# Kernel tuning notes

Measured on AMD Instinct MI355X. Metric: run time of the kernel, lower is better.

## Reference

```python
import jax, jax.numpy as jnp
import numpy as np

FEATURE_DIM = 256
NUM_STEPS = 3
NUM_GRAPHS = 2048
ATOMS_PER_GRAPH = 64
TOTAL_ATOMS = NUM_GRAPHS * ATOMS_PER_GRAPH


def setup_inputs() -> dict:
    key = jax.random.key(0)
    k_x, k1, k2, k3, k4 = jax.random.split(key, 5)
    H = FEATURE_DIM
    s = 1.0 / np.sqrt(H)
    x = jax.random.normal(k_x, (TOTAL_ATOMS, H), dtype=jnp.float32)
    batch = jnp.repeat(jnp.arange(NUM_GRAPHS, dtype=jnp.int64), ATOMS_PER_GRAPH)
    sizes = jnp.full((NUM_GRAPHS,), ATOMS_PER_GRAPH, dtype=jnp.int64)
    # LSTM params (PyTorch layout: gates ordered i, f, g, o)
    W_ih = jax.random.uniform(k1, (4 * H, H), jnp.float32, -s, s)
    W_hh = jax.random.uniform(k2, (4 * H, H), jnp.float32, -s, s)
    b_ih = jax.random.uniform(k3, (4 * H,), jnp.float32, -s, s)
    b_hh = jax.random.uniform(k4, (4 * H,), jnp.float32, -s, s)
    return {"x": x, "batch": batch, "sizes": sizes,
            "W_ih": W_ih, "W_hh": W_hh, "b_ih": b_ih, "b_hh": b_hh}


def _lstm_cell(u, hx, cx, W_ih, W_hh, b_ih, b_hh):
    # u: input [B,H]; (hx, cx): hidden/cell [B,H]
    gates = u @ W_ih.T + b_ih + hx @ W_hh.T + b_hh  # [B, 4H]
    i, f, g, o = jnp.split(gates, 4, axis=-1)
    i, f, o = jax.nn.sigmoid(i), jax.nn.sigmoid(f), jax.nn.sigmoid(o)
    c = f * cx + i * jnp.tanh(g)
    h = o * jnp.tanh(c)
    return h, c


def _segment_softmax(scores, seg, num_segments):
    m = jax.ops.segment_max(scores, seg, num_segments=num_segments)
    e = jnp.exp(scores - m[seg])
    s = jax.ops.segment_sum(e, seg, num_segments=num_segments)
    return e / s[seg]


def reference(x, batch, sizes, W_ih, W_hh, b_ih, b_hh):
    B = sizes.shape[0]
    H = x.shape[1]
    seg = batch.astype(jnp.int32)
    h = jnp.zeros((B, H), dtype=x.dtype)
    c = jnp.zeros((B, H), dtype=x.dtype)
    q = h
    r = h
    for _ in range(NUM_STEPS):
        # torch code feeds h both as LSTM input and hidden state
        q, c = _lstm_cell(h, h, c, W_ih, W_hh, b_ih, b_hh)
        scores = jnp.sum(x * q[seg], axis=-1)              # [total_atoms]
        attn = _segment_softmax(scores, seg, B)            # per-graph softmax
        r = jax.ops.segment_sum(x * attn[:, None], seg, num_segments=B)  # [B,H]
        h = r  # torch code overwrites the LSTM hidden with r
    return jnp.concatenate([q, r], axis=-1)  # [B, 2H]
```

## Files before the change

kernel.cpp:

```cpp
#include <hip/hip_runtime.h>
#include <math.h>

#define H 256
#define NB 2048
#define APG 64

typedef __attribute__((ext_vector_type(8))) short short8;
typedef __attribute__((ext_vector_type(4))) float f32x4;

__device__ __forceinline__ unsigned short f2bf(float f) {
    unsigned u = __float_as_uint(f);
    u += 0x7fff + ((u >> 16) & 1);
    return (unsigned short)(u >> 16);
}
__device__ __forceinline__ float bf2f(unsigned short s) {
    return __uint_as_float((unsigned)s << 16);
}
__device__ __forceinline__ float sigm(float v) { return 1.f / (1.f + __expf(-v)); }

__global__ void prep_kernel(const float* __restrict__ W_ih, const float* __restrict__ W_hh,
                            const float* __restrict__ b_ih, const float* __restrict__ b_hh,
                            unsigned short* __restrict__ Wr, float* __restrict__ br) {
    int idx = blockIdx.x * 256 + threadIdx.x;
    int wr_row = idx >> 8, k = idx & 255;
    int hcol = wr_row >> 2, gate = wr_row & 3;
    int src = gate * 65536 + hcol * 256 + k;
    Wr[idx] = f2bf(W_ih[src] + W_hh[src]);
    if (idx < 1024) {
        int hc = idx >> 2, gt = idx & 3;
        br[idx] = b_ih[gt * 256 + hc] + b_hh[gt * 256 + hc];
    }
}

__global__ __launch_bounds__(256)
void lstm0b(const float* __restrict__ br, float* __restrict__ q1,
            float* __restrict__ cbuf) {
    int g = blockIdx.x, t = threadIdx.x;
    float4 b4 = *(const float4*)&br[t * 4];
    float cn1 = sigm(b4.x) * tanhf(b4.z);
    cbuf[(size_t)g * H + t] = cn1;
    if (g == 0) q1[t] = sigm(b4.w) * tanhf(cn1);
}

__global__ __launch_bounds__(256)
void gemm_lstm(const unsigned short* __restrict__ hbf, const unsigned short* __restrict__ Wr,
               const float* __restrict__ br, float* __restrict__ c,
               float* __restrict__ qdst, int qstride) {
    __shared__ unsigned short smem[2][64 * 128];
    unsigned short* As = smem[0];
    unsigned short* Bs = smem[1];
    int t = threadIdx.x;
    int r0 = blockIdx.y * 64;
    int w0 = blockIdx.x * 64;
    int c0h = blockIdx.x * 16;
    int lane = t & 63, w = t >> 6;
    int ln = lane & 15, qd = lane >> 4;
    int m0 = w * 16;
    f32x4 acc[4] = {};
    for (int kc = 0; kc < 2; ++kc) {
        #pragma unroll
        for (int p = 0; p < 4; ++p) {
            int gid = p * 256 + t;
            int row = gid >> 4, g = gid & 15;
            int sg = g ^ (row & 15);
            *(short8*)&As[row * 128 + sg * 8] =
                *(const short8*)&hbf[(r0 + row) * H + kc * 128 + g * 8];
            *(short8*)&Bs[row * 128 + sg * 8] =
                *(const short8*)&Wr[(w0 + row) * H + kc * 128 + g * 8];
        }
        __syncthreads();
        #pragma unroll
        for (int kk = 0; kk < 4; ++kk) {
            int ga = (kk * 4 + qd) ^ ln;
            short8 a = *(short8*)&As[(m0 + ln) * 128 + ga * 8];
            #pragma unroll
            for (int t4 = 0; t4 < 4; ++t4) {
                short8 b = *(short8*)&Bs[(t4 * 16 + ln) * 128 + ga * 8];
                acc[t4] = __builtin_amdgcn_mfma_f32_16x16x32_bf16(a, b, acc[t4], 0, 0, 0);
            }
        }
        __syncthreads();
    }
    float* gl = (float*)smem;
    #pragma unroll
    for (int t4 = 0; t4 < 4; ++t4)
        #pragma unroll
        for (int r = 0; r < 4; ++r)
            gl[(m0 + qd * 4 + r) * 68 + t4 * 16 + ln] = acc[t4][r];
    __syncthreads();
    #pragma unroll
    for (int p = 0; p < 4; ++p) {
        int idx = p * 256 + t;
        int row = idx >> 4, hc = idx & 15;
        float4 g4 = *(float4*)&gl[row * 68 + hc * 4];
        float4 b4 = *(const float4*)&br[(c0h + hc) * 4];
        float gi = g4.x + b4.x, gf = g4.y + b4.y, gg = g4.z + b4.z, go = g4.w + b4.w;
        float si = sigm(gi), sf = sigm(gf), so = sigm(go);
        int cidx = (r0 + row) * H + c0h + hc;
        float cn = sf * c[cidx] + si * tanhf(gg);
        c[cidx] = cn;
        qdst[(r0 + row) * qstride + c0h + hc] = so * tanhf(cn);
    }
}

__global__ __launch_bounds__(256)
void attn(const float* __restrict__ x, const float* __restrict__ qsrc, int qstride,
          unsigned short* __restrict__ hbf_out, float* __restrict__ rout, int rstride) {
    __shared__ __align__(16) unsigned short xl[APG * H];
    __shared__ float sc[64];
    __shared__ float pl[64];
    __shared__ __align__(16) float rpart[4][256];
    int g = blockIdx.x, t = threadIdx.x;
    int lane = t & 63, w = t >> 6;
    const float* xg = x + (size_t)g * APG * H;

    float4 q4 = *(const float4*)&qsrc[(size_t)g * qstride + lane * 4];

    #pragma unroll
    for (int i = 0; i < 16; ++i) {
        int row = i * 4 + w;
        float4 f = *(const float4*)&xg[row * H + lane * 4];
        ushort4 u;
        u.x = f2bf(f.x); u.y = f2bf(f.y); u.z = f2bf(f.z); u.w = f2bf(f.w);
        *(ushort4*)&xl[row * H + lane * 4] = u;
        float p = f.x * q4.x + f.y * q4.y + f.z * q4.z + f.w * q4.w;
        #pragma unroll
        for (int d = 32; d > 0; d >>= 1) p += __shfl_xor(p, d, 64);
        if (lane == 0) sc[row] = p;
    }
    __syncthreads();

    if (t < 64) {
        float s = sc[t], m = s;
        #pragma unroll
        for (int d = 32; d > 0; d >>= 1) m = fmaxf(m, __shfl_xor(m, d, 64));
        float e = __expf(s - m), sum = e;
        #pragma unroll
        for (int d = 32; d > 0; d >>= 1) sum += __shfl_xor(sum, d, 64);
        pl[t] = e / sum;
    }
    __syncthreads();

    float4 r4 = {0.f, 0.f, 0.f, 0.f};
    #pragma unroll
    for (int i = 0; i < 16; ++i) {
        int row = i * 4 + w;
        float p = pl[row];
        ushort4 u = *(ushort4*)&xl[row * H + lane * 4];
        r4.x += p * bf2f(u.x); r4.y += p * bf2f(u.y);
        r4.z += p * bf2f(u.z); r4.w += p * bf2f(u.w);
    }
    *(float4*)&rpart[w][lane * 4] = r4;
    __syncthreads();
    float o = rpart[0][t] + rpart[1][t] + rpart[2][t] + rpart[3][t];
    if (hbf_out) hbf_out[(size_t)g * H + t] = f2bf(o);
    if (rout)    rout[(size_t)g * rstride + t] = o;
}

extern "C" void kernel_launch(void* const* d_in, const int* in_sizes, int n_in,
                              void* d_out, int out_size, void* d_ws, size_t ws_size,
                              hipStream_t stream) {
    const float* x    = (const float*)d_in[0];
    const float* W_ih = (const float*)d_in[3];
    const float* W_hh = (const float*)d_in[4];
    const float* b_ih = (const float*)d_in[5];
    const float* b_hh = (const float*)d_in[6];
    float* out = (float*)d_out;

    char* ws = (char*)d_ws;
    unsigned short* Wr   = (unsigned short*)ws;
    float*          br   = (float*)(ws + 524288);
    float*          q1   = (float*)(ws + 528384);
    float*          cbuf = (float*)(ws + 532480);
    float*          qbuf = (float*)(ws + 2629632);
    unsigned short* hbf  = (unsigned short*)(ws + 4726784);

    prep_kernel<<<1024, 256, 0, stream>>>(W_ih, W_hh, b_ih, b_hh, Wr, br);
    lstm0b<<<2048, 256, 0, stream>>>(br, q1, cbuf);
    attn<<<2048, 256, 0, stream>>>(x, q1, 0, hbf, nullptr, 0);
    gemm_lstm<<<dim3(16, 32), 256, 0, stream>>>(hbf, Wr, br, cbuf, qbuf, 256);
    attn<<<2048, 256, 0, stream>>>(x, qbuf, 256, hbf, nullptr, 0);
    gemm_lstm<<<dim3(16, 32), 256, 0, stream>>>(hbf, Wr, br, cbuf, out, 512);
    attn<<<2048, 256, 0, stream>>>(x, out, 512, nullptr, out + 256, 512);
}
```

Measured before the change: 267.8 us.

## Drop LDS bf16 staging in attention, fuse step-one LSTM into prep

The attention kernel no longer converts x to bf16 and stages it in 32KB of LDS. It re-reads the fp32 x rows from global memory (likely an L2 hit) for the weighted sum, and broadcasts the softmax weights via wave shuffles instead of a shared array plus a barrier. The per-graph constant first-step cell state is computed once inside the prep kernel instead of by a separate 2048-block kernel, and the first gemm reads it with stride 0. The last gemm skips writing the cell state. This cuts LDS use (raising occupancy), one launch and redundant writes, at the cost of a second global read of x per block.

```diff
diff --git a/kernel.cpp b/kernel.cpp
--- a/kernel.cpp
+++ b/kernel.cpp
@@ -13,39 +13,35 @@
     u += 0x7fff + ((u >> 16) & 1);
     return (unsigned short)(u >> 16);
 }
-__device__ __forceinline__ float bf2f(unsigned short s) {
-    return __uint_as_float((unsigned)s << 16);
-}
 __device__ __forceinline__ float sigm(float v) { return 1.f / (1.f + __expf(-v)); }
 
 __global__ void prep_kernel(const float* __restrict__ W_ih, const float* __restrict__ W_hh,
                             const float* __restrict__ b_ih, const float* __restrict__ b_hh,
-                            unsigned short* __restrict__ Wr, float* __restrict__ br) {
+                            unsigned short* __restrict__ Wr, float* __restrict__ br,
+                            float* __restrict__ q1, float* __restrict__ c1) {
     int idx = blockIdx.x * 256 + threadIdx.x;
     int wr_row = idx >> 8, k = idx & 255;
     int hcol = wr_row >> 2, gate = wr_row & 3;
     int src = gate * 65536 + hcol * 256 + k;
     Wr[idx] = f2bf(W_ih[src] + W_hh[src]);
-    if (idx < 1024) {
-        int hc = idx >> 2, gt = idx & 3;
-        br[idx] = b_ih[gt * 256 + hc] + b_hh[gt * 256 + hc];
+    if (blockIdx.x == 0) {
+        int t = threadIdx.x;
+        float bi  = b_ih[t]       + b_hh[t];
+        float bf_ = b_ih[256 + t] + b_hh[256 + t];
+        float bg  = b_ih[512 + t] + b_hh[512 + t];
+        float bo  = b_ih[768 + t] + b_hh[768 + t];
+        br[t * 4 + 0] = bi; br[t * 4 + 1] = bf_;
+        br[t * 4 + 2] = bg; br[t * 4 + 3] = bo;
+        float cn1 = sigm(bi) * tanhf(bg);
+        c1[t] = cn1;
+        q1[t] = sigm(bo) * tanhf(cn1);
     }
 }
 
 __global__ __launch_bounds__(256)
-void lstm0b(const float* __restrict__ br, float* __restrict__ q1,
-            float* __restrict__ cbuf) {
-    int g = blockIdx.x, t = threadIdx.x;
-    float4 b4 = *(const float4*)&br[t * 4];
-    float cn1 = sigm(b4.x) * tanhf(b4.z);
-    cbuf[(size_t)g * H + t] = cn1;
-    if (g == 0) q1[t] = sigm(b4.w) * tanhf(cn1);
-}
-
-__global__ __launch_bounds__(256)
 void gemm_lstm(const unsigned short* __restrict__ hbf, const unsigned short* __restrict__ Wr,
-               const float* __restrict__ br, float* __restrict__ c,
-               float* __restrict__ qdst, int qstride) {
+               const float* __restrict__ br, const float* __restrict__ cin, int cins,
+               float* __restrict__ cout, float* __restrict__ qdst, int qstride) {
     __shared__ unsigned short smem[2][64 * 128];
     unsigned short* As = smem[0];
     unsigned short* Bs = smem[1];
@@ -96,9 +92,9 @@
         float4 b4 = *(const float4*)&br[(c0h + hc) * 4];
         float gi = g4.x + b4.x, gf = g4.y + b4.y, gg = g4.z + b4.z, go = g4.w + b4.w;
         float si = sigm(gi), sf = sigm(gf), so = sigm(go);
-        int cidx = (r0 + row) * H + c0h + hc;
-        float cn = sf * c[cidx] + si * tanhf(gg);
-        c[cidx] = cn;
+        float cprev = cin[(r0 + row) * cins + c0h + hc];
+        float cn = sf * cprev + si * tanhf(gg);
+        if (cout) cout[(r0 + row) * H + c0h + hc] = cn;
         qdst[(r0 + row) * qstride + c0h + hc] = so * tanhf(cn);
     }
 }
@@ -106,9 +102,7 @@
 __global__ __launch_bounds__(256)
 void attn(const float* __restrict__ x, const float* __restrict__ qsrc, int qstride,
           unsigned short* __restrict__ hbf_out, float* __restrict__ rout, int rstride) {
-    __shared__ __align__(16) unsigned short xl[APG * H];
     __shared__ float sc[64];
-    __shared__ float pl[64];
     __shared__ __align__(16) float rpart[4][256];
     int g = blockIdx.x, t = threadIdx.x;
     int lane = t & 63, w = t >> 6;
@@ -120,9 +114,6 @@
     for (int i = 0; i < 16; ++i) {
         int row = i * 4 + w;
         float4 f = *(const float4*)&xg[row * H + lane * 4];
-        ushort4 u;
-        u.x = f2bf(f.x); u.y = f2bf(f.y); u.z = f2bf(f.z); u.w = f2bf(f.w);
-        *(ushort4*)&xl[row * H + lane * 4] = u;
         float p = f.x * q4.x + f.y * q4.y + f.z * q4.z + f.w * q4.w;
         #pragma unroll
         for (int d = 32; d > 0; d >>= 1) p += __shfl_xor(p, d, 64);
@@ -130,25 +121,21 @@
     }
     __syncthreads();
 
-    if (t < 64) {
-        float s = sc[t], m = s;
-        #pragma unroll
-        for (int d = 32; d > 0; d >>= 1) m = fmaxf(m, __shfl_xor(m, d, 64));
-        float e = __expf(s - m), sum = e;
-        #pragma unroll
-        for (int d = 32; d > 0; d >>= 1) sum += __shfl_xor(sum, d, 64);
-        pl[t] = e / sum;
-    }
-    __syncthreads();
+    float sv = sc[lane], m = sv;
+    #pragma unroll
+    for (int d = 32; d > 0; d >>= 1) m = fmaxf(m, __shfl_xor(m, d, 64));
+    float e = __expf(sv - m), sum = e;
+    #pragma unroll
+    for (int d = 32; d > 0; d >>= 1) sum += __shfl_xor(sum, d, 64);
+    float pv = e / sum;
 
     float4 r4 = {0.f, 0.f, 0.f, 0.f};
     #pragma unroll
     for (int i = 0; i < 16; ++i) {
         int row = i * 4 + w;
-        float p = pl[row];
-        ushort4 u = *(ushort4*)&xl[row * H + lane * 4];
-        r4.x += p * bf2f(u.x); r4.y += p * bf2f(u.y);
-        r4.z += p * bf2f(u.z); r4.w += p * bf2f(u.w);
+        float p = __shfl(pv, row, 64);
+        float4 f = *(const float4*)&xg[row * H + lane * 4];
+        r4.x += p * f.x; r4.y += p * f.y; r4.z += p * f.z; r4.w += p * f.w;
     }
     *(float4*)&rpart[w][lane * 4] = r4;
     __syncthreads();
@@ -171,15 +158,15 @@
     unsigned short* Wr   = (unsigned short*)ws;
     float*          br   = (float*)(ws + 524288);
     float*          q1   = (float*)(ws + 528384);
+    float*          c1   = (float*)(ws + 529408);
     float*          cbuf = (float*)(ws + 532480);
     float*          qbuf = (float*)(ws + 2629632);
     unsigned short* hbf  = (unsigned short*)(ws + 4726784);
 
-    prep_kernel<<<1024, 256, 0, stream>>>(W_ih, W_hh, b_ih, b_hh, Wr, br);
-    lstm0b<<<2048, 256, 0, stream>>>(br, q1, cbuf);
+    prep_kernel<<<1024, 256, 0, stream>>>(W_ih, W_hh, b_ih, b_hh, Wr, br, q1, c1);
     attn<<<2048, 256, 0, stream>>>(x, q1, 0, hbf, nullptr, 0);
-    gemm_lstm<<<dim3(16, 32), 256, 0, stream>>>(hbf, Wr, br, cbuf, qbuf, 256);
+    gemm_lstm<<<dim3(16, 32), 256, 0, stream>>>(hbf, Wr, br, c1, 0, cbuf, qbuf, 256);
     attn<<<2048, 256, 0, stream>>>(x, qbuf, 256, hbf, nullptr, 0);
-    gemm_lstm<<<dim3(16, 32), 256, 0, stream>>>(hbf, Wr, br, cbuf, out, 512);
+    gemm_lstm<<<dim3(16, 32), 256, 0, stream>>>(hbf, Wr, br, cbuf, 256, nullptr, out, 512);
     attn<<<2048, 256, 0, stream>>>(x, out, 512, nullptr, out + 256, 512);
 }
```

Result: slower. 302.4 us (+12.9%).
